# Performance work log

Hardware: AMD Instinct MI355X
Metric: run time of the kernel (lower is better)

## Reference

```python
import jax, jax.numpy as jnp
import numpy as np

EP = 1e-4
EPMAX = 30.0
RTOL, ATOL = 1e-5, 1e-8  # torch.allclose defaults


def _safe(n):
    return jnp.where(n == 0, 1.0, n)


def _rigid_from_3(x):
    # x: (L, 3, 3) -> rot (L,3,3) rows e1,e2,e3 ; origin (L,3)
    x1, x2, x3 = x[:, 0], x[:, 1], x[:, 2]
    v1 = x3 - x2
    v2 = x1 - x2
    e1 = v1 / (jnp.linalg.norm(v1, axis=-1, keepdims=True) + 1e-3)
    u2 = v2 - e1 * jnp.einsum('ld,ld->l', e1, v2)[:, None]
    e2 = u2 / (jnp.linalg.norm(u2, axis=-1, keepdims=True) + 1e-8)
    e3 = jnp.cross(e1, e2)
    return jnp.stack([e1, e2, e3], axis=1), x2


def _merge_frames(rot, trans, ii, jj):
    # Vectorized merge_coordinate_systems over all selected pairs (ii, jj).
    O_A, O_B = trans[ii], trans[jj]          # (P,3)
    RA, RB = rot[ii], rot[jj]                # (P,3,3)
    close = jnp.all(jnp.abs(O_A - O_B) <= ATOL + RTOL * jnp.abs(O_B), axis=-1)
    d = O_B - O_A
    nd = jnp.linalg.norm(d, axis=-1)
    X_new = d / _safe(nd)[:, None]
    Z_add = RA[:, 2] + RB[:, 2]
    Z_sub = RA[:, 2] - RB[:, 2]
    na = jnp.linalg.norm(Z_add, axis=-1)
    ns = jnp.linalg.norm(Z_sub, axis=-1)
    Z_new = jnp.where((na > ns)[:, None], Z_add / _safe(na)[:, None], Z_sub / _safe(ns)[:, None])
    Y_new = jnp.cross(Z_new, X_new)
    nan_bad = jnp.any(jnp.isnan(Y_new), axis=-1)
    flip = jnp.einsum('pd,pd->p', jnp.cross(X_new, Y_new), Z_new) < 0
    Y_new = jnp.where(flip[:, None], -Y_new, Y_new)
    R_new = jnp.stack([X_new, Y_new, Z_new], axis=1)  # (P,3,3)
    O_new = 0.5 * (O_A + O_B)
    bad = close | (nd == 0) | (na == 0) | (ns == 0) | nan_bad
    R_out = jnp.where(bad[:, None, None], RA, R_new)
    O_out = jnp.where(bad[:, None], O_A, O_new)
    return jnp.concatenate([rot, R_out], axis=0), jnp.concatenate([trans, O_out], axis=0)


def _frame_transform(points, rot, tran):
    # points: (N,3); rot: (F,3,3); tran: (F,3) -> (N,F,3)
    diff = points[:, None, :] - tran[None, :, :]
    return jnp.einsum('nfd,fed->nfe', diff, rot)


def setup_inputs():
    key = jax.random.key(0)
    k0, k1, k2, k3 = jax.random.split(key, 4)
    L = 1024
    coor = 5.0 * jax.random.normal(k0, (L, 3, 3), jnp.float32)
    # valid orthonormal frames from random points
    rot, _ = _rigid_from_3(5.0 * jax.random.normal(k1, (L, 3, 3), jnp.float32))
    trans = 5.0 * jax.random.normal(k2, (L, 3), jnp.float32)
    target = 5.0 * jax.random.normal(k3, (L, 3, 3), jnp.float32)
    idx = np.arange(L)
    band = idx[None, :] - idx[:, None]
    matrix = ((band > 0) & (band <= 8)).astype(np.int32)  # ~8k contact pairs
    return {"coor": coor, "rot": rot, "trans": trans, "target": target,
            "matrix": jnp.asarray(matrix)}


def reference(coor, rot, trans, target, matrix):
    m = np.asarray(matrix)
    ii_np, jj_np = np.nonzero(np.triu(m, 1) == 1)
    ii, jj = jnp.asarray(ii_np), jnp.asarray(jj_np)
    p_rot, p_tran = _merge_frames(rot, trans, ii, jj)
    pred_x2 = _frame_transform(coor.reshape(-1, 3), p_rot, p_tran)   # (N,F,3)
    t_rot0, t_tran0 = _rigid_from_3(target)
    t_rot, t_tran = _merge_frames(t_rot0, t_tran0, ii, jj)
    tx = _frame_transform(target.reshape(-1, 3), t_rot, t_tran)     # (N,F,3)
    errmap = jnp.sqrt(jnp.sum((pred_x2 - tx) ** 2 + EP, axis=-1))
    return jnp.mean(jnp.minimum(errmap, EPMAX))
```

## Files before the change

kernel.cpp:

```cpp
#include <hip/hip_runtime.h>

#define EPV    0.0001f
#define EPMAXV 30.0f
#define CHUNK  64
#define NPART  2048


__global__ void k_prep(const int* __restrict__ m, int L, unsigned int* __restrict__ rowcnt,
                       const float* __restrict__ rot, const float* __restrict__ trans,
                       const float* __restrict__ target, int nrb,
                       float* __restrict__ pF, float* __restrict__ tF) {
    if ((int)blockIdx.x < nrb) {
        int i = blockIdx.x * 4 + (threadIdx.x >> 6);
        if (i >= L) return;
        int lane = threadIdx.x & 63;
        const int* row = m + (size_t)i * L;
        unsigned int c = 0;
        for (int j0 = 0; j0 < L; j0 += 64) {
            int j = j0 + lane;
            bool v = (j < L) && (j > i) && (row[j] == 1);
            unsigned long long b = __ballot(v);
            c += (unsigned int)__popcll(b);
        }
        if (lane == 0) rowcnt[i] = c;
        return;
    }
    int l = ((int)blockIdx.x - nrb) * 256 + threadIdx.x;
    if (l >= L) return;
    float* pf = pF + l * 12;
#pragma unroll
    for (int k = 0; k < 9; k++) pf[k] = rot[l * 9 + k];
    pf[9]  = trans[l * 3 + 0];
    pf[10] = trans[l * 3 + 1];
    pf[11] = trans[l * 3 + 2];
    const float* tg = target + l * 9;
    float x1x = tg[0], x1y = tg[1], x1z = tg[2];
    float x2x = tg[3], x2y = tg[4], x2z = tg[5];
    float x3x = tg[6], x3y = tg[7], x3z = tg[8];
    float v1x = x3x - x2x, v1y = x3y - x2y, v1z = x3z - x2z;
    float v2x = x1x - x2x, v2y = x1y - x2y, v2z = x1z - x2z;
    float n1 = sqrtf(v1x * v1x + v1y * v1y + v1z * v1z) + 0.001f;
    float e1x = v1x / n1, e1y = v1y / n1, e1z = v1z / n1;
    float c = e1x * v2x + e1y * v2y + e1z * v2z;
    float u2x = v2x - c * e1x, u2y = v2y - c * e1y, u2z = v2z - c * e1z;
    float n2 = sqrtf(u2x * u2x + u2y * u2y + u2z * u2z) + 1e-8f;
    float e2x = u2x / n2, e2y = u2y / n2, e2z = u2z / n2;
    float e3x = e1y * e2z - e1z * e2y;
    float e3y = e1z * e2x - e1x * e2z;
    float e3z = e1x * e2y - e1y * e2x;
    float* tf = tF + l * 12;
    tf[0] = e1x; tf[1] = e1y; tf[2] = e1z;
    tf[3] = e2x; tf[4] = e2y; tf[5] = e2z;
    tf[6] = e3x; tf[7] = e3y; tf[8] = e3z;
    tf[9] = x2x; tf[10] = x2y; tf[11] = x2z;
}

#define RTOLV  1e-5f
#define ATOLV  1e-8f

__device__ inline void merge_frames(const float* __restrict__ A, const float* __restrict__ B,
                                    float* __restrict__ out) {
    const float* RA = A; const float* OA = A + 9;
    const float* RB = B; const float* OB = B + 9;
    bool close = (fabsf(OA[0] - OB[0]) <= ATOLV + RTOLV * fabsf(OB[0])) &&
                 (fabsf(OA[1] - OB[1]) <= ATOLV + RTOLV * fabsf(OB[1])) &&
                 (fabsf(OA[2] - OB[2]) <= ATOLV + RTOLV * fabsf(OB[2]));
    float d0 = OB[0] - OA[0], d1 = OB[1] - OA[1], d2 = OB[2] - OA[2];
    float nd = sqrtf(d0 * d0 + d1 * d1 + d2 * d2);
    float nds = (nd == 0.f) ? 1.f : nd;
    float X0 = d0 / nds, X1 = d1 / nds, X2 = d2 / nds;
    float Za0 = RA[6] + RB[6], Za1 = RA[7] + RB[7], Za2 = RA[8] + RB[8];
    float Zs0 = RA[6] - RB[6], Zs1 = RA[7] - RB[7], Zs2 = RA[8] - RB[8];
    float na = sqrtf(Za0 * Za0 + Za1 * Za1 + Za2 * Za2);
    float ns = sqrtf(Zs0 * Zs0 + Zs1 * Zs1 + Zs2 * Zs2);
    float nas = (na == 0.f) ? 1.f : na;
    float nss = (ns == 0.f) ? 1.f : ns;
    float Z0, Z1, Z2;
    if (na > ns) { Z0 = Za0 / nas; Z1 = Za1 / nas; Z2 = Za2 / nas; }
    else         { Z0 = Zs0 / nss; Z1 = Zs1 / nss; Z2 = Zs2 / nss; }
    float Y0 = Z1 * X2 - Z2 * X1;
    float Y1 = Z2 * X0 - Z0 * X2;
    float Y2 = Z0 * X1 - Z1 * X0;
    bool nanbad = (Y0 != Y0) || (Y1 != Y1) || (Y2 != Y2);
    float C0 = X1 * Y2 - X2 * Y1;
    float C1 = X2 * Y0 - X0 * Y2;
    float C2 = X0 * Y1 - X1 * Y0;
    float dotv = C0 * Z0 + C1 * Z1 + C2 * Z2;
    if (dotv < 0.f) { Y0 = -Y0; Y1 = -Y1; Y2 = -Y2; }
    bool bad = close || (nd == 0.f) || (na == 0.f) || (ns == 0.f) || nanbad;
    if (bad) {
#pragma unroll
        for (int k = 0; k < 12; k++) out[k] = A[k];
    } else {
        out[0] = X0; out[1] = X1; out[2] = X2;
        out[3] = Y0; out[4] = Y1; out[5] = Y2;
        out[6] = Z0; out[7] = Z1; out[8] = Z2;
        out[9]  = 0.5f * (OA[0] + OB[0]);
        out[10] = 0.5f * (OA[1] + OB[1]);
        out[11] = 0.5f * (OA[2] + OB[2]);
    }
}

__global__ void k_fillmerge(const int* __restrict__ m, int L,
                            const unsigned int* __restrict__ rowcnt,
                            unsigned int* __restrict__ count, int cap,
                            float* __restrict__ pF, float* __restrict__ tF) {
    int i = blockIdx.x * 4 + (threadIdx.x >> 6);
    int lane = threadIdx.x & 63;

    if (blockIdx.x == 0 && (threadIdx.x >> 6) == 0) {
        unsigned int t = 0;
        for (int r = lane; r < L; r += 64) t += rowcnt[r];
#pragma unroll
        for (int off = 1; off < 64; off <<= 1) t += __shfl_xor(t, off, 64);
        if (lane == 0) *count = t;
    }
    if (i >= L) return;

    unsigned int p = 0;
    for (int r = lane; r < i; r += 64) p += rowcnt[r];
#pragma unroll
    for (int off = 1; off < 64; off <<= 1) p += __shfl_xor(p, off, 64);
    unsigned int base = p;

    const int* row = m + (size_t)i * L;
    unsigned long long lt = (lane == 0) ? 0ull : ((1ull << lane) - 1ull);
    for (int j0 = 0; j0 < L; j0 += 64) {
        int j = j0 + lane;
        bool v = (j < L) && (j > i) && (row[j] == 1);
        unsigned long long b = __ballot(v);
        if (v) {
            unsigned int pos = base + (unsigned int)__popcll(b & lt);
            if (pos < (unsigned int)cap) {
                merge_frames(pF + i * 12, pF + j * 12, pF + (size_t)(L + pos) * 12);
                merge_frames(tF + i * 12, tF + j * 12, tF + (size_t)(L + pos) * 12);
            }
        }
        base += (unsigned int)__popcll(b);
    }
}

__global__ __launch_bounds__(256)
void k_main(const float* __restrict__ coor, const float* __restrict__ target,
            const float* __restrict__ pF, const float* __restrict__ tF,
            const unsigned int* __restrict__ count, int cap, int L, int Npts,
            double* __restrict__ partials) {
    __shared__ float4 sC[CHUNK];
    __shared__ float4 sT[CHUNK];
    __shared__ float sRed[4];
    unsigned int cnt = *count;
    if (cnt > (unsigned int)cap) cnt = (unsigned int)cap;
    int F = L + (int)cnt;
    int nfb = (F + 255) >> 8;
    int nyc = (Npts + CHUNK - 1) / CHUNK;
    int total = nfb * nyc;
    float a0 = 0.f, a1 = 0.f;

    for (int chunk = blockIdx.x; chunk < total; chunk += gridDim.x) {
        int fb = chunk % nfb;
        int yc = chunk / nfb;
        int n0 = yc * CHUNK;
        int npts = Npts - n0; if (npts > CHUNK) npts = CHUNK;
        __syncthreads();
        for (int idx = threadIdx.x; idx < npts; idx += 256) {
            int g = (n0 + idx) * 3;
            sC[idx] = make_float4(coor[g], coor[g + 1], coor[g + 2], 0.f);
            sT[idx] = make_float4(target[g], target[g + 1], target[g + 2], 0.f);
        }
        __syncthreads();
        int f = fb * 256 + threadIdx.x;
        if (f >= F) continue;

        const float4* pf4 = (const float4*)(pF + (size_t)f * 12);
        const float4* tf4 = (const float4*)(tF + (size_t)f * 12);
        float4 p0 = pf4[0], p1 = pf4[1], p2 = pf4[2];
        float4 t0 = tf4[0], t1 = tf4[1], t2 = tf4[2];
        float P00 = p0.x, P01 = p0.y, P02 = p0.z;
        float P10 = p0.w, P11 = p1.x, P12 = p1.y;
        float P20 = p1.z, P21 = p1.w, P22 = p2.x;
        float tPx = p2.y, tPy = p2.z, tPz = p2.w;
        float T00 = t0.x, T01 = t0.y, T02 = t0.z;
        float T10 = t0.w, T11 = t1.x, T12 = t1.y;
        float T20 = t1.z, T21 = t1.w, T22 = t2.x;
        float tTx = t2.y, tTy = t2.z, tTz = t2.w;
        float kx = T00 * tTx + T01 * tTy + T02 * tTz - (P00 * tPx + P01 * tPy + P02 * tPz);
        float ky = T10 * tTx + T11 * tTy + T12 * tTz - (P10 * tPx + P11 * tPy + P12 * tPz);
        float kz = T20 * tTx + T21 * tTy + T22 * tTz - (P20 * tPx + P21 * tPy + P22 * tPz);
        float N00 = -T00, N01 = -T01, N02 = -T02;
        float N10 = -T10, N11 = -T11, N12 = -T12;
        float N20 = -T20, N21 = -T21, N22 = -T22;

#pragma unroll 4
        for (int n = 0; n < npts; n++) {
            float4 c = sC[n];
            float4 t = sT[n];
            float ux = kx + P00 * c.x + P01 * c.y + P02 * c.z
                          + N00 * t.x + N01 * t.y + N02 * t.z;
            float uy = ky + P10 * c.x + P11 * c.y + P12 * c.z
                          + N10 * t.x + N11 * t.y + N12 * t.z;
            float uz = kz + P20 * c.x + P21 * c.y + P22 * c.z
                          + N20 * t.x + N21 * t.y + N22 * t.z;
            float s = ux * ux + uy * uy + uz * uz + 3.0f * EPV;
            float r = fminf(sqrtf(s), EPMAXV);
            if (n & 1) a1 += r; else a0 += r;
        }
    }

    float a = a0 + a1;
#pragma unroll
    for (int off = 32; off > 0; off >>= 1) a += __shfl_down(a, off, 64);
    int lane = threadIdx.x & 63, wv = threadIdx.x >> 6;
    if (lane == 0) sRed[wv] = a;
    __syncthreads();
    if (threadIdx.x == 0)
        partials[blockIdx.x] = (double)(sRed[0] + sRed[1] + sRed[2] + sRed[3]);
}

__global__ void k_final(const double* __restrict__ partials, int npart,
                        const unsigned int* __restrict__ count, int cap,
                        int L, int Npts, float* __restrict__ out) {
    __shared__ double sR[4];
    double d = 0.0;
    for (int i = threadIdx.x; i < npart; i += 256) d += partials[i];
#pragma unroll
    for (int off = 32; off > 0; off >>= 1) d += __shfl_down(d, off, 64);
    int lane = threadIdx.x & 63, wv = threadIdx.x >> 6;
    if (lane == 0) sR[wv] = d;
    __syncthreads();
    if (threadIdx.x == 0) {
        double tot = sR[0] + sR[1] + sR[2] + sR[3];
        unsigned int cnt = *count;
        if (cnt > (unsigned int)cap) cnt = (unsigned int)cap;
        double F = (double)(L + (int)cnt);
        out[0] = (float)(tot / ((double)Npts * F));
    }
}

extern "C" void kernel_launch(void* const* d_in, const int* in_sizes, int n_in,
                              void* d_out, int out_size, void* d_ws, size_t ws_size,
                              hipStream_t stream) {
    const float* coor   = (const float*)d_in[0];
    const float* rot    = (const float*)d_in[1];
    const float* trans  = (const float*)d_in[2];
    const float* target = (const float*)d_in[3];
    const int*   matrix = (const int*)d_in[4];
    int L    = in_sizes[2] / 3;
    int Npts = 3 * L;

    char* ws = (char*)d_ws;
    size_t off = 16;
    unsigned int* count  = (unsigned int*)ws;
    unsigned int* rowcnt = (unsigned int*)(ws + off); off += 4 * (size_t)L;
    off = (off + 15) & ~(size_t)15;
    double* partials = (double*)(ws + off); off += 8 * (size_t)NPART;
    off = (off + 15) & ~(size_t)15;
    long cap_ws = ((long)ws_size - (long)off - 96L * (long)L) / 96;
    long capl = cap_ws < 32768 ? cap_ws : 32768;
    if (capl < 0) capl = 0;
    int cap = (int)(capl & ~1L);
    float* pF = (float*)(ws + off);
    float* tF = pF + (size_t)(L + cap) * 12;

    int nrb   = (L + 3) / 4;
    int nbase = (L + 255) / 256;
    k_prep<<<nrb + nbase, 256, 0, stream>>>(matrix, L, rowcnt, rot, trans, target,
                                            nrb, pF, tF);
    k_fillmerge<<<nrb, 256, 0, stream>>>(matrix, L, rowcnt, count, cap, pF, tF);
    k_main<<<NPART, 256, 0, stream>>>(coor, target, pF, tF, count, cap, L, Npts, partials);
    k_final<<<1, 256, 0, stream>>>(partials, NPART, count, cap, L, Npts, (float*)d_out);
}
```

Measured before the change: 114.8 us.

## Precompute fused per-frame records and loop frames per point thread

After: 116.7 us. Within noise of the previous version (+1.6%).

```diff
diff --git a/kernel.cpp b/kernel.cpp
--- a/kernel.cpp
+++ b/kernel.cpp
@@ -2,14 +2,38 @@
 
 #define EPV    0.0001f
 #define EPMAXV 30.0f
-#define CHUNK  64
+#define RTOLV  1e-5f
+#define ATOLV  1e-8f
 #define NPART  2048
-
+#define FS     64
+
+
+__device__ inline void write_rec(float* __restrict__ rec,
+                                 const float Rp[9], const float Op[3],
+                                 const float Rt[9], const float Ot[3]) {
+    float P[9], N[9];
+#pragma unroll
+    for (int k = 0; k < 9; k++) { P[k] = Rp[k]; N[k] = -Rt[k]; }
+    float kx = -(P[0] * Op[0] + P[1] * Op[1] + P[2] * Op[2]
+               + N[0] * Ot[0] + N[1] * Ot[1] + N[2] * Ot[2]);
+    float ky = -(P[3] * Op[0] + P[4] * Op[1] + P[5] * Op[2]
+               + N[3] * Ot[0] + N[4] * Ot[1] + N[5] * Ot[2]);
+    float kz = -(P[6] * Op[0] + P[7] * Op[1] + P[8] * Op[2]
+               + N[6] * Ot[0] + N[7] * Ot[1] + N[8] * Ot[2]);
+    float4* r4 = (float4*)rec;
+    r4[0] = make_float4(P[0], P[1], P[2], P[3]);
+    r4[1] = make_float4(P[4], P[5], P[6], P[7]);
+    r4[2] = make_float4(P[8], N[0], N[1], N[2]);
+    r4[3] = make_float4(N[3], N[4], N[5], N[6]);
+    r4[4] = make_float4(N[7], N[8], kx, ky);
+    r4[5] = make_float4(kz, 0.f, 0.f, 0.f);
+}
 
 __global__ void k_prep(const int* __restrict__ m, int L, unsigned int* __restrict__ rowcnt,
                        const float* __restrict__ rot, const float* __restrict__ trans,
                        const float* __restrict__ target, int nrb,
-                       float* __restrict__ pF, float* __restrict__ tF) {
+                       float* __restrict__ pF, float* __restrict__ tF,
+                       float* __restrict__ rec) {
     if ((int)blockIdx.x < nrb) {
         int i = blockIdx.x * 4 + (threadIdx.x >> 6);
         if (i >= L) return;
@@ -27,12 +51,16 @@
     }
     int l = ((int)blockIdx.x - nrb) * 256 + threadIdx.x;
     if (l >= L) return;
+    float Rp[9], Op[3];
+#pragma unroll
+    for (int k = 0; k < 9; k++) Rp[k] = rot[l * 9 + k];
+#pragma unroll
+    for (int k = 0; k < 3; k++) Op[k] = trans[l * 3 + k];
     float* pf = pF + l * 12;
 #pragma unroll
-    for (int k = 0; k < 9; k++) pf[k] = rot[l * 9 + k];
-    pf[9]  = trans[l * 3 + 0];
-    pf[10] = trans[l * 3 + 1];
-    pf[11] = trans[l * 3 + 2];
+    for (int k = 0; k < 9; k++) pf[k] = Rp[k];
+#pragma unroll
+    for (int k = 0; k < 3; k++) pf[9 + k] = Op[k];
     const float* tg = target + l * 9;
     float x1x = tg[0], x1y = tg[1], x1z = tg[2];
     float x2x = tg[3], x2y = tg[4], x2z = tg[5];
@@ -45,21 +73,23 @@
     float u2x = v2x - c * e1x, u2y = v2y - c * e1y, u2z = v2z - c * e1z;
     float n2 = sqrtf(u2x * u2x + u2y * u2y + u2z * u2z) + 1e-8f;
     float e2x = u2x / n2, e2y = u2y / n2, e2z = u2z / n2;
-    float e3x = e1y * e2z - e1z * e2y;
-    float e3y = e1z * e2x - e1x * e2z;
-    float e3z = e1x * e2y - e1y * e2x;
+    float Rt[9], Ot[3];
+    Rt[0] = e1x; Rt[1] = e1y; Rt[2] = e1z;
+    Rt[3] = e2x; Rt[4] = e2y; Rt[5] = e2z;
+    Rt[6] = e1y * e2z - e1z * e2y;
+    Rt[7] = e1z * e2x - e1x * e2z;
+    Rt[8] = e1x * e2y - e1y * e2x;
+    Ot[0] = x2x; Ot[1] = x2y; Ot[2] = x2z;
     float* tf = tF + l * 12;
-    tf[0] = e1x; tf[1] = e1y; tf[2] = e1z;
-    tf[3] = e2x; tf[4] = e2y; tf[5] = e2z;
-    tf[6] = e3x; tf[7] = e3y; tf[8] = e3z;
-    tf[9] = x2x; tf[10] = x2y; tf[11] = x2z;
-}
-
-#define RTOLV  1e-5f
-#define ATOLV  1e-8f
+#pragma unroll
+    for (int k = 0; k < 9; k++) tf[k] = Rt[k];
+#pragma unroll
+    for (int k = 0; k < 3; k++) tf[9 + k] = Ot[k];
+    write_rec(rec + (size_t)l * 24, Rp, Op, Rt, Ot);
+}
 
 __device__ inline void merge_frames(const float* __restrict__ A, const float* __restrict__ B,
-                                    float* __restrict__ out) {
+                                    float R[9], float O[3]) {
     const float* RA = A; const float* OA = A + 9;
     const float* RB = B; const float* OB = B + 9;
     bool close = (fabsf(OA[0] - OB[0]) <= ATOLV + RTOLV * fabsf(OB[0])) &&
@@ -90,21 +120,24 @@
     bool bad = close || (nd == 0.f) || (na == 0.f) || (ns == 0.f) || nanbad;
     if (bad) {
 #pragma unroll
-        for (int k = 0; k < 12; k++) out[k] = A[k];
+        for (int k = 0; k < 9; k++) R[k] = RA[k];
+#pragma unroll
+        for (int k = 0; k < 3; k++) O[k] = OA[k];
     } else {
-        out[0] = X0; out[1] = X1; out[2] = X2;
-        out[3] = Y0; out[4] = Y1; out[5] = Y2;
-        out[6] = Z0; out[7] = Z1; out[8] = Z2;
-        out[9]  = 0.5f * (OA[0] + OB[0]);
-        out[10] = 0.5f * (OA[1] + OB[1]);
-        out[11] = 0.5f * (OA[2] + OB[2]);
+        R[0] = X0; R[1] = X1; R[2] = X2;
+        R[3] = Y0; R[4] = Y1; R[5] = Y2;
+        R[6] = Z0; R[7] = Z1; R[8] = Z2;
+        O[0] = 0.5f * (OA[0] + OB[0]);
+        O[1] = 0.5f * (OA[1] + OB[1]);
+        O[2] = 0.5f * (OA[2] + OB[2]);
     }
 }
 
 __global__ void k_fillmerge(const int* __restrict__ m, int L,
                             const unsigned int* __restrict__ rowcnt,
                             unsigned int* __restrict__ count, int cap,
-                            float* __restrict__ pF, float* __restrict__ tF) {
+                            const float* __restrict__ pF, const float* __restrict__ tF,
+                            float* __restrict__ rec) {
     int i = blockIdx.x * 4 + (threadIdx.x >> 6);
     int lane = threadIdx.x & 63;
 
@@ -132,8 +165,10 @@
         if (v) {
             unsigned int pos = base + (unsigned int)__popcll(b & lt);
             if (pos < (unsigned int)cap) {
-                merge_frames(pF + i * 12, pF + j * 12, pF + (size_t)(L + pos) * 12);
-                merge_frames(tF + i * 12, tF + j * 12, tF + (size_t)(L + pos) * 12);
+                float Rp[9], Op[3], Rt[9], Ot[3];
+                merge_frames(pF + i * 12, pF + j * 12, Rp, Op);
+                merge_frames(tF + i * 12, tF + j * 12, Rt, Ot);
+                write_rec(rec + (size_t)(L + pos) * 24, Rp, Op, Rt, Ot);
             }
         }
         base += (unsigned int)__popcll(b);
@@ -142,68 +177,42 @@
 
 __global__ __launch_bounds__(256)
 void k_main(const float* __restrict__ coor, const float* __restrict__ target,
-            const float* __restrict__ pF, const float* __restrict__ tF,
-            const unsigned int* __restrict__ count, int cap, int L, int Npts,
-            double* __restrict__ partials) {
-    __shared__ float4 sC[CHUNK];
-    __shared__ float4 sT[CHUNK];
+            const float* __restrict__ rec, const unsigned int* __restrict__ count,
+            int cap, int L, int Npts, double* __restrict__ partials) {
     __shared__ float sRed[4];
     unsigned int cnt = *count;
     if (cnt > (unsigned int)cap) cnt = (unsigned int)cap;
     int F = L + (int)cnt;
-    int nfb = (F + 255) >> 8;
-    int nyc = (Npts + CHUNK - 1) / CHUNK;
-    int total = nfb * nyc;
+    int npb = (Npts + 255) >> 8;
+    int nfs = (F + FS - 1) / FS;
+    int total = npb * nfs;
     float a0 = 0.f, a1 = 0.f;
 
     for (int chunk = blockIdx.x; chunk < total; chunk += gridDim.x) {
-        int fb = chunk % nfb;
-        int yc = chunk / nfb;
-        int n0 = yc * CHUNK;
-        int npts = Npts - n0; if (npts > CHUNK) npts = CHUNK;
-        __syncthreads();
-        for (int idx = threadIdx.x; idx < npts; idx += 256) {
-            int g = (n0 + idx) * 3;
-            sC[idx] = make_float4(coor[g], coor[g + 1], coor[g + 2], 0.f);
-            sT[idx] = make_float4(target[g], target[g + 1], target[g + 2], 0.f);
+        int pb = chunk % npb;
+        int fsI = chunk / npb;
+        int pt = pb * 256 + threadIdx.x;
+        bool alive = pt < Npts;
+        int pi = alive ? pt * 3 : 0;
+        float cx = coor[pi],   cy = coor[pi + 1],   cz = coor[pi + 2];
+        float tx = target[pi], ty = target[pi + 1], tz = target[pi + 2];
+        int f0 = fsI * FS;
+        int f1 = f0 + FS; if (f1 > F) f1 = F;
+        float b0 = 0.f, b1 = 0.f;
+#pragma unroll 2
+        for (int f = f0; f < f1; f++) {
+            const float* fr = rec + (size_t)f * 24;
+            float ux = fr[18] + fr[0] * cx + fr[1] * cy + fr[2] * cz
+                               + fr[9] * tx + fr[10] * ty + fr[11] * tz;
+            float uy = fr[19] + fr[3] * cx + fr[4] * cy + fr[5] * cz
+                               + fr[12] * tx + fr[13] * ty + fr[14] * tz;
+            float uz = fr[20] + fr[6] * cx + fr[7] * cy + fr[8] * cz
+                               + fr[15] * tx + fr[16] * ty + fr[17] * tz;
+            float s = ux * ux + uy * uy + uz * uz + 3.0f * EPV;
+            float r = fminf(__builtin_amdgcn_sqrtf(s), EPMAXV);
+            if (f & 1) b1 += r; else b0 += r;
         }
-        __syncthreads();
-        int f = fb * 256 + threadIdx.x;
-        if (f >= F) continue;
-
-        const float4* pf4 = (const float4*)(pF + (size_t)f * 12);
-        const float4* tf4 = (const float4*)(tF + (size_t)f * 12);
-        float4 p0 = pf4[0], p1 = pf4[1], p2 = pf4[2];
-        float4 t0 = tf4[0], t1 = tf4[1], t2 = tf4[2];
-        float P00 = p0.x, P01 = p0.y, P02 = p0.z;
-        float P10 = p0.w, P11 = p1.x, P12 = p1.y;
-        float P20 = p1.z, P21 = p1.w, P22 = p2.x;
-        float tPx = p2.y, tPy = p2.z, tPz = p2.w;
-        float T00 = t0.x, T01 = t0.y, T02 = t0.z;
-        float T10 = t0.w, T11 = t1.x, T12 = t1.y;
-        float T20 = t1.z, T21 = t1.w, T22 = t2.x;
-        float tTx = t2.y, tTy = t2.z, tTz = t2.w;
-        float kx = T00 * tTx + T01 * tTy + T02 * tTz - (P00 * tPx + P01 * tPy + P02 * tPz);
-        float ky = T10 * tTx + T11 * tTy + T12 * tTz - (P10 * tPx + P11 * tPy + P12 * tPz);
-        float kz = T20 * tTx + T21 * tTy + T22 * tTz - (P20 * tPx + P21 * tPy + P22 * tPz);
-        float N00 = -T00, N01 = -T01, N02 = -T02;
-        float N10 = -T10, N11 = -T11, N12 = -T12;
-        float N20 = -T20, N21 = -T21, N22 = -T22;
-
-#pragma unroll 4
-        for (int n = 0; n < npts; n++) {
-            float4 c = sC[n];
-            float4 t = sT[n];
-            float ux = kx + P00 * c.x + P01 * c.y + P02 * c.z
-                          + N00 * t.x + N01 * t.y + N02 * t.z;
-            float uy = ky + P10 * c.x + P11 * c.y + P12 * c.z
-                          + N10 * t.x + N11 * t.y + N12 * t.z;
-            float uz = kz + P20 * c.x + P21 * c.y + P22 * c.z
-                          + N20 * t.x + N21 * t.y + N22 * t.z;
-            float s = ux * ux + uy * uy + uz * uz + 3.0f * EPV;
-            float r = fminf(sqrtf(s), EPMAXV);
-            if (n & 1) a1 += r; else a0 += r;
-        }
+        if (alive) { a0 += b0; a1 += b1; }
     }
 
     float a = a0 + a1;
@@ -254,18 +263,20 @@
     off = (off + 15) & ~(size_t)15;
     double* partials = (double*)(ws + off); off += 8 * (size_t)NPART;
     off = (off + 15) & ~(size_t)15;
+    float* pF = (float*)(ws + off); off += 48 * (size_t)L;
+    float* tF = (float*)(ws + off); off += 48 * (size_t)L;
+    off = (off + 15) & ~(size_t)15;
     long cap_ws = ((long)ws_size - (long)off - 96L * (long)L) / 96;
     long capl = cap_ws < 32768 ? cap_ws : 32768;
     if (capl < 0) capl = 0;
-    int cap = (int)(capl & ~1L);
-    float* pF = (float*)(ws + off);
-    float* tF = pF + (size_t)(L + cap) * 12;
+    int cap = (int)capl;
+    float* rec = (float*)(ws + off);
 
     int nrb   = (L + 3) / 4;
     int nbase = (L + 255) / 256;
     k_prep<<<nrb + nbase, 256, 0, stream>>>(matrix, L, rowcnt, rot, trans, target,
-                                            nrb, pF, tF);
-    k_fillmerge<<<nrb, 256, 0, stream>>>(matrix, L, rowcnt, count, cap, pF, tF);
-    k_main<<<NPART, 256, 0, stream>>>(coor, target, pF, tF, count, cap, L, Npts, partials);
+                                            nrb, pF, tF, rec);
+    k_fillmerge<<<nrb, 256, 0, stream>>>(matrix, L, rowcnt, count, cap, pF, tF, rec);
+    k_main<<<NPART, 256, 0, stream>>>(coor, target, rec, count, cap, L, Npts, partials);
     k_final<<<1, 256, 0, stream>>>(partials, NPART, count, cap, L, Npts, (float*)d_out);
 }
```
